# Kernel optimization log

Measured on AMD Instinct MI355X. Metric: run time of the kernel, lower is better.

## Reference

```python
import jax, jax.numpy as jnp
import numpy as np
from jax import lax

K = 3      # kernel_size
C = 64     # n_feat
B, H, W = 2, 256, 256


def _conv(x, w, b, pad):
    # NCHW conv, stride 1
    out = lax.conv_general_dilated(x, w, (1, 1), [(pad, pad), (pad, pad)],
                                   dimension_numbers=('NCHW', 'OIHW', 'NCHW'))
    return out + b[None, :, None, None]


def _prelu(x, a):
    # nn.PReLU() with a single shared learnable slope (init 0.25)
    return jnp.where(x >= 0, x, a * x)


def setup_inputs():
    key = jax.random.key(0)
    ks = jax.random.split(key, 20)
    s = 0.05
    def w(k, shape):
        return jax.random.normal(k, shape, jnp.float32) * s
    inp = {
        'image': jax.random.normal(ks[0], (B, C, H, W), jnp.float32),
        'guidance': jax.random.normal(ks[1], (B, C, H, W), jnp.float32),
        # self.tensor: 1x1 conv (2C -> C) + PReLU (shared with jbf_conv's act)
        'tensor_w': w(ks[2], (C, 2 * C, 1, 1)),
        'tensor_b': jnp.zeros((C,), jnp.float32),
        'a_jbf': jnp.full((1,), 0.25, jnp.float32),
        'kg_w1': w(ks[3], (C, C, 3, 3)), 'kg_b1': jnp.zeros((C,), jnp.float32),
        'kg_w2': w(ks[4], (C, C, 3, 3)), 'kg_b2': jnp.zeros((C,), jnp.float32),
        'kg_w3': w(ks[5], (C, C, 3, 3)), 'kg_b3': jnp.zeros((C,), jnp.float32),
        'kg_w4': w(ks[6], (C, C, 3, 3)), 'kg_b4': jnp.zeros((C,), jnp.float32),
        'kg_w5': w(ks[7], (K * K * C, C, 1, 1)),
        'kg_b5': jnp.zeros((K * K * C,), jnp.float32),
        'a_kg': jnp.full((1,), 0.25, jnp.float32),
        # jbf_conv: 3x3 C->C, PReLU (shared a_jbf), 3x3 C->C
        'jbf_w1': w(ks[8], (C, C, 3, 3)), 'jbf_b1': jnp.zeros((C,), jnp.float32),
        'jbf_w2': w(ks[9], (C, C, 3, 3)), 'jbf_b2': jnp.zeros((C,), jnp.float32),
    }
    return inp


def reference(image, guidance, tensor_w, tensor_b, a_jbf,
              kg_w1, kg_b1, kg_w2, kg_b2, kg_w3, kg_b3, kg_w4, kg_b4,
              kg_w5, kg_b5, a_kg, jbf_w1, jbf_b1, jbf_w2, jbf_b2):
    b, c, h, w = image.shape
    # fuse target+guidance features
    t = _prelu(_conv(jnp.concatenate([image, guidance], axis=1), tensor_w, tensor_b, 0), a_jbf)
    # concat_kg: predict per-pixel dynamic kernel (b, K*K*c, h, w)
    y = t
    for wt, bs in ((kg_w1, kg_b1), (kg_w2, kg_b2), (kg_w3, kg_b3), (kg_w4, kg_b4)):
        y = _prelu(_conv(y, wt, bs, 1), a_kg)
    bi_kernel = _conv(y, kg_w5, kg_b5, 0)
    # unfold: torch layout is channel-major (c, ki, kj) along dim 1
    p = (K - 1) // 2
    xp = jnp.pad(image, ((0, 0), (0, 0), (p, p), (p, p)))
    taps = [xp[:, :, i:i + h, j:j + w] for i in range(K) for j in range(K)]
    patch = jnp.stack(taps, axis=2).reshape(b, c * K * K, h, w)
    # NOTE: faithful to source -- (c*K*K) flat layout reinterpreted as (K*K, c)
    jbf = (patch * bi_kernel).reshape(b, K * K, c, h, w).sum(axis=1)
    out = _conv(_prelu(_conv(jbf, jbf_w1, jbf_b1, 1), a_jbf), jbf_w2, jbf_b2, 1)
    return out + image
```

## Files before the change

kernel.cpp:

```cpp
#include <hip/hip_runtime.h>

#define HW 65536

typedef __bf16 bf16x8 __attribute__((ext_vector_type(8)));
typedef float f32x16 __attribute__((ext_vector_type(16)));

__device__ inline unsigned short f2bf(float x) {
    union { float f; unsigned u; } v; v.f = x;
    unsigned r = v.u + 0x7FFF + ((v.u >> 16) & 1);
    return (unsigned short)(r >> 16);
}
__device__ inline float bfhi2f(unsigned u) {
    union { unsigned u; float f; } v; v.u = u & 0xffff0000u; return v.f;
}
__device__ inline float bflo2f(unsigned u) {
    union { unsigned u; float f; } v; v.u = u << 16; return v.f;
}

union FragU { uint4 u; bf16x8 v; };
__device__ inline bf16x8 ld_frag(const uint4* p) { FragU t; t.u = *p; return t.v; }


__global__ __launch_bounds__(256) void k_pre(
    const float* __restrict__ img, const float* __restrict__ gd,
    const float* __restrict__ w0, const float* __restrict__ w1,
    const float* __restrict__ w2, const float* __restrict__ w3,
    const float* __restrict__ w4, const float* __restrict__ w5,
    const float* __restrict__ w5c, const float* __restrict__ tw,
    unsigned short* __restrict__ imgT, unsigned short* __restrict__ gdT,
    unsigned short* __restrict__ wT)
{
    __shared__ float sT[64 * 66];
    int tid = threadIdx.x;
    int y = blockIdx.y;
    if (y < 4) {
        int z = y;
        int b = z & 1;
        const float* src = (z >> 1) ? gd : img;
        unsigned short* dst = (z >> 1) ? gdT : imgT;
        int px0 = blockIdx.x * 64;
        size_t sbase = (size_t)b * 64 * HW + px0;

#pragma unroll
        for (int i = 0; i < 4; ++i) {
            int e = i * 256 + tid;
            int ic = e >> 4, seg = e & 15;
            float4 v = *(const float4*)(src + sbase + (size_t)ic * HW + seg * 4);
            float* p = &sT[ic * 66 + seg * 4];
            ((float2*)p)[0] = make_float2(v.x, v.y);
            ((float2*)p)[1] = make_float2(v.z, v.w);
        }
        __syncthreads();

        size_t dbase = (size_t)b * HW * 64 + (size_t)px0 * 64;
#pragma unroll
        for (int k = 0; k < 2; ++k) {
            int idx = k * 256 + tid;
            int px = idx >> 3, u = idx & 7;
            union { uint4 q; unsigned short h[8]; } o;
#pragma unroll
            for (int j = 0; j < 8; ++j)
                o.h[j] = f2bf(sT[(u * 8 + j) * 66 + px]);
            *(uint4*)(dst + dbase + (size_t)px * 64 + u * 8) = o.q;
        }
    } else {
        int y2 = y - 4;
        unsigned short* o = wT + (size_t)y2 * 36864;
        int e = blockIdx.x * 256 + tid;
        if (y2 < 6) {
            const float* ws_[6] = {w0, w1, w2, w3, w4, w5};
            const float* w = ws_[y2];
            if (e < 36864) {
                int tap = e >> 12, oc = (e >> 6) & 63, ic = e & 63;
                int igg = ic >> 3, j = ic & 7;
                int dst = ((tap * 8 + igg) * 64 + oc) * 8 + j;
                o[dst] = f2bf(w[(oc * 64 + ic) * 9 + tap]);
            }
        } else if (y2 == 6) {
            if (e < 36864) o[e] = f2bf(w5c[e]);
        } else {
            if (e < 8192) {
                int oc = e >> 7, ic = e & 127;
                int kg = ic >> 3, j = ic & 7;
                o[((kg * 64 + oc) << 3) + j] = f2bf(tw[e]);
            }
        }
    }
}

__global__ __launch_bounds__(256, 2) void k_fuse3(
    const unsigned short* __restrict__ imgT, const unsigned short* __restrict__ gdT,
    const unsigned short* __restrict__ wTf,
    const unsigned short* __restrict__ w1T, const unsigned short* __restrict__ w2T,
    const float* __restrict__ tb, const float* __restrict__ b1,
    const float* __restrict__ b2, const float* __restrict__ ajbf,
    const float* __restrict__ akg, unsigned short* __restrict__ out)
{
    __shared__ __align__(16) char smem[54528];
    float* sB = (float*)(smem + 53760);
    uint4* sS0 = (uint4*)smem;
    uint4* sS1 = (uint4*)(smem + 19200);

    int tid = threadIdx.x;
    int wv = tid >> 6, lane = tid & 63;
    int half = lane >> 5, l31 = lane & 31;
    int w2 = wv >> 1, g = wv & 1;
    int lin = blockIdx.x + (blockIdx.y << 4) + (blockIdx.z << 9);
    int slab = lin & 7, sub = lin >> 3;
    int b = slab >> 2;
    int y0 = (slab & 3) * 64 + (sub >> 4) * 8;
    int x0 = (sub & 15) * 16;
    const size_t zbase = (size_t)b * HW * 64;
    const uint4* wgf = (const uint4*)wTf;
    const uint4* wg1 = (const uint4*)w1T;
    const uint4* wg2 = (const uint4*)w2T;

    if (tid < 64) sB[tid] = tb[tid];
    else if (tid < 128) sB[tid] = b1[tid - 64];
    else if (tid < 192) sB[tid] = b2[tid - 128];

    auto loadS = [&](int t, int h, uint4* rx) {
        const unsigned short* src = t ? gdT : imgT;
#pragma unroll
        for (int i = 0; i < 4; ++i) {
            int e = i * 256 + tid;
            int cell = e >> 2, ig = e & 3;
            int r = cell / 20, c2 = cell - r * 20;
            int gy = y0 - 2 + r, gx = x0 - 2 + c2;
            rx[i] = make_uint4(0, 0, 0, 0);
            if (e < 960 && gy >= 0 && gy < 256 && gx >= 0 && gx < 256)
                rx[i] = *(const uint4*)(src + zbase + ((size_t)(gy * 256 + gx)) * 64 + h * 32 + ig * 8);
        }
    };
    auto writeS = [&](uint4* s, const uint4* rx) {
#pragma unroll
        for (int i = 0; i < 4; ++i) {
            int e = i * 256 + tid;
            if (e < 960) s[(e >> 2) * 5 + (e & 3)] = rx[i];
        }
    };

    int cell0[4];
#pragma unroll
    for (int s = 0; s < 4; ++s) {
        int c = g * 128 + s * 32 + l31;
        cell0[s] = c < 240 ? c : 239;
    }
    f32x16 acc0[4];
#pragma unroll
    for (int s = 0; s < 4; ++s)
#pragma unroll
        for (int r = 0; r < 16; ++r) acc0[s][r] = 0.f;

    auto mm1 = [&](int t, int h, const uint4* sS) {
#pragma unroll
        for (int c = 0; c < 2; ++c) {
            int ig = c * 2 + half;
            int kg = t * 8 + h * 4 + ig;
            bf16x8 af = ld_frag(&wgf[kg * 64 + w2 * 32 + l31]);
#pragma unroll
            for (int s = 0; s < 4; ++s) {
                bf16x8 bb = ld_frag(&sS[cell0[s] * 5 + ig]);
                acc0[s] = __builtin_amdgcn_mfma_f32_32x32x16_bf16(af, bb, acc0[s], 0, 0, 0);
            }
        }
    };

    uint4 rx[4];
    loadS(0, 0, rx);
    writeS(sS0, rx);
    loadS(0, 1, rx);
    __syncthreads();
    mm1(0, 0, sS0);
    writeS(sS1, rx);
    loadS(1, 0, rx);
    __syncthreads();
    mm1(0, 1, sS1);
    writeS(sS0, rx);
    loadS(1, 1, rx);
    __syncthreads();
    mm1(1, 0, sS0);
    writeS(sS1, rx);
    __syncthreads();
    mm1(1, 1, sS1);

    float s_jbf = ajbf[0], s_kg = akg[0];
    __syncthreads();
    unsigned short* sC0 = (unsigned short*)smem;
#pragma unroll
    for (int s = 0; s < 4; ++s) {
        int cell = g * 128 + s * 32 + l31;
        if (cell < 240) {
            int R = cell / 20, C = cell - R * 20;
            int gy = y0 - 2 + R, gx = x0 - 2 + C;
            bool inb = (gy >= 0 && gy < 256 && gx >= 0 && gx < 256);
#pragma unroll
            for (int q2 = 0; q2 < 4; ++q2) {
                unsigned short hw[4];
#pragma unroll
                for (int j = 0; j < 4; ++j) {
                    int r = (q2 << 2) | j;
                    int oc = w2 * 32 + j + 8 * q2 + 4 * half;
                    float v = acc0[s][r] + sB[oc];
                    v = (v >= 0.f) ? v : s_jbf * v;
                    if (!inb) v = 0.f;
                    hw[j] = f2bf(v);
                }
                int up = (w2 * 4 + q2) ^ (cell & 7);
                *(uint2*)&sC0[cell * 64 + up * 8 + half * 4] =
                    make_uint2((unsigned)hw[0] | ((unsigned)hw[1] << 16),
                               (unsigned)hw[2] | ((unsigned)hw[3] << 16));
            }
        }
    }
    __syncthreads();

    int cellv[3], ibv[3];
#pragma unroll
    for (int s = 0; s < 3; ++s) {
        int c = g * 96 + s * 32 + l31;
        cellv[s] = c;
        int cc = c < 180 ? c : 179;
        ibv[s] = (cc / 18) * 20 + (cc % 18);
    }
    f32x16 acc1[3];
#pragma unroll
    for (int s = 0; s < 3; ++s)
#pragma unroll
        for (int r = 0; r < 16; ++r) acc1[s][r] = 0.f;

    {
        const uint4* sC04 = (const uint4*)smem;
#pragma unroll
        for (int dy = 0; dy < 3; ++dy) {
#pragma unroll
            for (int dx = 0; dx < 3; ++dx) {
                int tap = dy * 3 + dx;
                int doff = dy * 20 + dx;
#pragma unroll
                for (int c4 = 0; c4 < 4; ++c4) {
                    int unit = c4 * 2 + half;
                    bf16x8 af = ld_frag(&wg1[(tap * 8 + unit) * 64 + w2 * 32 + l31]);
#pragma unroll
                    for (int s = 0; s < 3; ++s) {
                        int cc = ibv[s] + doff;
                        bf16x8 bb = ld_frag(&sC04[cc * 8 + (unit ^ (cc & 7))]);
                        acc1[s] = __builtin_amdgcn_mfma_f32_32x32x16_bf16(af, bb, acc1[s], 0, 0, 0);
                    }
                }
            }
        }
    }

    unsigned short* sC1 = (unsigned short*)(smem + 30720);
#pragma unroll
    for (int s = 0; s < 3; ++s) {
        int cell = cellv[s];
        if (cell < 180) {
            int orow = cell / 18, ocol = cell - orow * 18;
            int gy = y0 - 1 + orow, gx = x0 - 1 + ocol;
            bool inb = (gy >= 0 && gy < 256 && gx >= 0 && gx < 256);
#pragma unroll
            for (int q2 = 0; q2 < 4; ++q2) {
                unsigned short hw[4];
#pragma unroll
                for (int j = 0; j < 4; ++j) {
                    int r = (q2 << 2) | j;
                    int oc = w2 * 32 + j + 8 * q2 + 4 * half;
                    float v = acc1[s][r] + sB[64 + oc];
                    v = (v >= 0.f) ? v : s_kg * v;
                    if (!inb) v = 0.f;
                    hw[j] = f2bf(v);
                }
                int up = (w2 * 4 + q2) ^ (cell & 7);
                *(uint2*)&sC1[cell * 64 + up * 8 + half * 4] =
                    make_uint2((unsigned)hw[0] | ((unsigned)hw[1] << 16),
                               (unsigned)hw[2] | ((unsigned)hw[3] << 16));
            }
        }
    }
    __syncthreads();

    f32x16 acc2[2];
#pragma unroll
    for (int s = 0; s < 2; ++s)
#pragma unroll
        for (int r = 0; r < 16; ++r) acc2[s][r] = 0.f;

    int rowS[2], colS[2];
#pragma unroll
    for (int s = 0; s < 2; ++s) {
        int px = g * 64 + s * 32 + l31;
        rowS[s] = px >> 4; colS[s] = px & 15;
    }
    {
        const uint4* sC14 = (const uint4*)(smem + 30720);
#pragma unroll
        for (int dy = 0; dy < 3; ++dy) {
#pragma unroll
            for (int dx = 0; dx < 3; ++dx) {
                int tap = dy * 3 + dx;
#pragma unroll
                for (int c = 0; c < 4; ++c) {
                    int ig = c * 2 + half;
                    bf16x8 af = ld_frag(&wg2[(tap * 8 + ig) * 64 + w2 * 32 + l31]);
#pragma unroll
                    for (int s = 0; s < 2; ++s) {
                        int cl = (rowS[s] + dy) * 18 + colS[s] + dx;
                        bf16x8 bb = ld_frag(&sC14[cl * 8 + (ig ^ (cl & 7))]);
                        acc2[s] = __builtin_amdgcn_mfma_f32_32x32x16_bf16(af, bb, acc2[s], 0, 0, 0);
                    }
                }
            }
        }
    }

    unsigned short* sT16 = (unsigned short*)smem;
#pragma unroll
    for (int s = 0; s < 2; ++s) {
        int px = g * 64 + s * 32 + l31;
#pragma unroll
        for (int q2 = 0; q2 < 4; ++q2) {
            unsigned short hw[4];
#pragma unroll
            for (int j = 0; j < 4; ++j) {
                int r = (q2 << 2) | j;
                int oc = w2 * 32 + j + 8 * q2 + 4 * half;
                float v = acc2[s][r] + sB[128 + oc];
                v = (v >= 0.f) ? v : s_kg * v;
                hw[j] = f2bf(v);
            }
            int up = (w2 * 4 + q2) ^ (px & 7);
            uint2* p = (uint2*)&sT16[px * 64 + up * 8 + half * 4];
            *p = make_uint2((unsigned)hw[0] | ((unsigned)hw[1] << 16),
                            (unsigned)hw[2] | ((unsigned)hw[3] << 16));
        }
    }
    __syncthreads();
#pragma unroll
    for (int k = 0; k < 4; ++k) {
        int idx = k * 256 + tid;
        int row = idx >> 7, rem = idx & 127;
        int col = rem >> 3, u = rem & 7;
        int px = row * 16 + col;
        uint4 v = *(uint4*)&sT16[px * 64 + (u ^ (px & 7)) * 8];
        *(uint4*)(out + zbase + ((size_t)((y0 + row) * 256 + x0 + col)) * 64 + u * 8) = v;
    }
}

#define XU 5

template<int MODE>
__global__ __launch_bounds__(256, 4) void k_conv2x(
    const unsigned short* __restrict__ in,
    const unsigned short* __restrict__ w1T, const unsigned short* __restrict__ w2T,
    const float* __restrict__ b1, const float* __restrict__ b2,
    const float* __restrict__ a, const float* __restrict__ res,
    void* __restrict__ outv)
{
    __shared__ __align__(16) char smem[38912];
    uint4* sIn0 = (uint4*)smem;
    uint4* sIn1 = (uint4*)(smem + 19200);
    float* sB = (float*)(smem + 38400);

    int tid = threadIdx.x;
    int wv = tid >> 6, lane = tid & 63;
    int half = lane >> 5, l31 = lane & 31;
    int w2 = wv >> 1, g = wv & 1;
    int lin = blockIdx.x + (blockIdx.y << 4) + (blockIdx.z << 9);
    int slab = lin & 7, sub = lin >> 3;
    int b = slab >> 2;
    int y0 = (slab & 3) * 64 + (sub >> 4) * 8;
    int x0 = (sub & 15) * 16;
    const size_t zbase = (size_t)b * HW * 64;
    const uint4* wg1 = (const uint4*)w1T;
    const uint4* wg2 = (const uint4*)w2T;

    if (tid < 64) sB[tid] = b1[tid];
    else if (tid < 128) sB[tid] = b2[tid - 64];

    auto loadIn = [&](int h, uint4* rx) {
#pragma unroll
        for (int i = 0; i < 4; ++i) {
            int e = i * 256 + tid;
            int cell = e >> 2, ig = e & 3;
            int r = cell / 20, c2 = cell - r * 20;
            int gy = y0 - 2 + r, gx = x0 - 2 + c2;
            rx[i] = make_uint4(0, 0, 0, 0);
            bool act = (i < 3) || (e < 960);
            if (act && gy >= 0 && gy < 256 && gx >= 0 && gx < 256)
                rx[i] = *(const uint4*)(in + zbase + ((size_t)(gy * 256 + gx)) * 64 + h * 32 + ig * 8);
        }
    };
    auto writeIn = [&](uint4* s, const uint4* rx) {
#pragma unroll
        for (int i = 0; i < 4; ++i) {
            int e = i * 256 + tid;
            if (i < 3 || e < 960) s[(e >> 2) * XU + (e & 3)] = rx[i];
        }
    };

    int cellv[3], ibv[3];
#pragma unroll
    for (int s = 0; s < 3; ++s) {
        int c = g * 96 + s * 32 + l31;
        cellv[s] = c;
        int cc = c < 180 ? c : 179;
        ibv[s] = (cc / 18) * 20 + (cc % 18);
    }

    f32x16 acc1[3];
#pragma unroll
    for (int s = 0; s < 3; ++s)
#pragma unroll
        for (int r = 0; r < 16; ++r) acc1[s][r] = 0.f;

    auto conv1_h = [&](int h, const uint4* sInp) {
#pragma unroll
        for (int dy = 0; dy < 3; ++dy) {
#pragma unroll
            for (int dx = 0; dx < 3; ++dx) {
                int tap = dy * 3 + dx;
                int doff = dy * 20 + dx;
#pragma unroll
                for (int c = 0; c < 2; ++c) {
                    int ig = c * 2 + half;
                    bf16x8 af = ld_frag(&wg1[(tap * 8 + h * 4 + ig) * 64 + w2 * 32 + l31]);
#pragma unroll
                    for (int s = 0; s < 3; ++s) {
                        bf16x8 bb = ld_frag(&sInp[(ibv[s] + doff) * XU + ig]);
                        acc1[s] = __builtin_amdgcn_mfma_f32_32x32x16_bf16(af, bb, acc1[s], 0, 0, 0);
                    }
                }
            }
        }
    };

    uint4 rx[4];
    loadIn(0, rx);
    writeIn(sIn0, rx);
    uint4 ry[4];
    loadIn(1, ry);
    __syncthreads();
    conv1_h(0, sIn0);
    writeIn(sIn1, ry);
    __syncthreads();
    conv1_h(1, sIn1);

    float s1 = a[0];
    __syncthreads();
    unsigned short* sC16 = (unsigned short*)smem;
#pragma unroll
    for (int s = 0; s < 3; ++s) {
        int cell = cellv[s];
        if (cell < 180) {
            int orow = cell / 18, ocol = cell - orow * 18;
            int gy = y0 - 1 + orow, gx = x0 - 1 + ocol;
            bool inb = (gy >= 0 && gy < 256 && gx >= 0 && gx < 256);
#pragma unroll
            for (int q2 = 0; q2 < 4; ++q2) {
                unsigned short hw[4];
#pragma unroll
                for (int j = 0; j < 4; ++j) {
                    int r = (q2 << 2) | j;
                    int oc = w2 * 32 + j + 8 * q2 + 4 * half;
                    float v = acc1[s][r] + sB[oc];
                    v = (v >= 0.f) ? v : s1 * v;
                    if (!inb) v = 0.f;
                    hw[j] = f2bf(v);
                }
                int up = (w2 * 4 + q2) ^ (cell & 7);
                *(uint2*)&sC16[cell * 64 + up * 8 + half * 4] =
                    make_uint2((unsigned)hw[0] | ((unsigned)hw[1] << 16),
                               (unsigned)hw[2] | ((unsigned)hw[3] << 16));
            }
        }
    }
    __syncthreads();

    f32x16 acc2[2];
#pragma unroll
    for (int s = 0; s < 2; ++s)
#pragma unroll
        for (int r = 0; r < 16; ++r) acc2[s][r] = 0.f;

    int rowS[2], colS[2];
#pragma unroll
    for (int s = 0; s < 2; ++s) {
        int px = g * 64 + s * 32 + l31;
        rowS[s] = px >> 4; colS[s] = px & 15;
    }
    {
        const uint4* sC4 = (const uint4*)smem;
#pragma unroll
        for (int dy = 0; dy < 3; ++dy) {
#pragma unroll
            for (int dx = 0; dx < 3; ++dx) {
                int tap = dy * 3 + dx;
#pragma unroll
                for (int c = 0; c < 4; ++c) {
                    int ig = c * 2 + half;
                    bf16x8 af = ld_frag(&wg2[(tap * 8 + ig) * 64 + w2 * 32 + l31]);
#pragma unroll
                    for (int s = 0; s < 2; ++s) {
                        int cl = (rowS[s] + dy) * 18 + colS[s] + dx;
                        bf16x8 bb = ld_frag(&sC4[cl * 8 + (ig ^ (cl & 7))]);
                        acc2[s] = __builtin_amdgcn_mfma_f32_32x32x16_bf16(af, bb, acc2[s], 0, 0, 0);
                    }
                }
            }
        }
    }

    if (MODE == 0) {
        __syncthreads();
        unsigned short* sT16 = (unsigned short*)smem;
#pragma unroll
        for (int s = 0; s < 2; ++s) {
            int px = g * 64 + s * 32 + l31;
#pragma unroll
            for (int q2 = 0; q2 < 4; ++q2) {
                unsigned short hw[4];
#pragma unroll
                for (int j = 0; j < 4; ++j) {
                    int r = (q2 << 2) | j;
                    int oc = w2 * 32 + j + 8 * q2 + 4 * half;
                    float v = acc2[s][r] + sB[64 + oc];
                    v = (v >= 0.f) ? v : s1 * v;
                    hw[j] = f2bf(v);
                }
                int up = (w2 * 4 + q2) ^ (px & 7);
                uint2* p = (uint2*)&sT16[px * 64 + up * 8 + half * 4];
                *p = make_uint2((unsigned)hw[0] | ((unsigned)hw[1] << 16),
                                (unsigned)hw[2] | ((unsigned)hw[3] << 16));
            }
        }
        __syncthreads();
        unsigned short* outT = (unsigned short*)outv;
#pragma unroll
        for (int k = 0; k < 4; ++k) {
            int idx = k * 256 + tid;
            int row = idx >> 7, rem = idx & 127;
            int col = rem >> 3, u = rem & 7;
            int px = row * 16 + col;
            uint4 v = *(uint4*)&sT16[px * 64 + (u ^ (px & 7)) * 8];
            *(uint4*)(outT + zbase + ((size_t)((y0 + row) * 256 + x0 + col)) * 64 + u * 8) = v;
        }
    } else {
        float* outF = (float*)outv;
#pragma unroll
        for (int s = 0; s < 2; ++s) {
            int px = g * 64 + s * 32 + l31;
            int y = y0 + (px >> 4), x = x0 + (px & 15);
            size_t pbase = (size_t)b * 64 * HW + (size_t)y * 256 + x;
#pragma unroll
            for (int r = 0; r < 16; ++r) {
                int oc = w2 * 32 + (r & 3) + 8 * (r >> 2) + 4 * half;
                float v = acc2[s][r] + sB[64 + oc];
                v += res[pbase + (size_t)oc * HW];
                outF[pbase + (size_t)oc * HW] = v;
            }
        }
    }
}

struct OffTab { unsigned v[9][32]; int chlo[9]; };
constexpr OffTab make_tab() {
    OffTab t{};
    for (int kk = 0; kk < 9; ++kk) {
        int chlo = (kk * 64) / 9;
        t.chlo[kk] = chlo;
        for (int ot = 0; ot < 2; ++ot)
            for (int r = 0; r < 16; ++r) {
                int cc0 = ot * 32 + (r & 3) + 8 * (r >> 2);
                int q0 = kk * 64 + cc0, q1 = q0 + 4;
                int o0 = (q0 / 9 - chlo) * 360 + (q0 % 9 / 3) * 40 + (q0 % 9 % 3);
                int o1 = (q1 / 9 - chlo) * 360 + (q1 % 9 / 3) * 40 + (q1 % 9 % 3);
                t.v[kk][ot * 16 + r] = (unsigned)o0 | ((unsigned)o1 << 16);
            }
    }
    return t;
}
__constant__ OffTab kOff = make_tab();

__global__ __launch_bounds__(256, 2) void k_jbfm(
    const unsigned short* __restrict__ y4, const float* __restrict__ img,
    const unsigned short* __restrict__ w5T, const float* __restrict__ b5,
    unsigned short* __restrict__ out)
{
    __shared__ __align__(16) char smem[78592];
    uint4* sY = (uint4*)smem;
    float* sB5 = (float*)(smem + 76288);
    unsigned short* sT16 = (unsigned short*)smem;

    int tid = threadIdx.x;
    int wv = tid >> 6, lane = tid & 63;
    int half = lane >> 5, l31 = lane & 31;
    int lin = blockIdx.x + (blockIdx.y << 3) + (blockIdx.z << 8);
    int slab = lin & 7, sub = lin >> 3;
    int b = slab >> 2;
    int y0 = (slab & 3) * 64 + (sub >> 3) * 8;
    int x0 = (sub & 7) * 32;
    size_t zbase = (size_t)b * HW * 64;
    size_t ibase = (size_t)b * 64 * HW;

    int p_off[3], p_dst[3];
    bool p_a[3], p_b[3], p_act[3];
#pragma unroll
    for (int i = 0; i < 3; ++i) {
        int e = i * 256 + tid;
        bool act = e < 720;
        int ch = e / 90, rem = e - ch * 90;
        int rp = rem / 10, seg = rem - rp * 10;
        int gy = y0 + rp - 1;
        int gxb = x0 - 4 + seg * 4;
        bool xok = (gxb >= 0 && gxb < 256);
        p_act[i] = act;
        p_a[i] = act && xok && gy >= 0 && gy < 256;
        p_b[i] = act && xok && (gy + 1) < 256;
        p_off[i] = ch * HW + gy * 256 + gxb;
        p_dst[i] = ch * 360 + rp * 40 + seg * 4;
    }

#pragma unroll
    for (int i = 0; i < 8; ++i) {
        int e = i * 256 + tid;
        int px = e >> 3, ig = e & 7;
        int gy = y0 + (px >> 5), gx = x0 + (px & 31);
        sY[px * 9 + ig] = *(const uint4*)(y4 + zbase + ((size_t)(gy * 256 + gx)) * 64 + ig * 8);
    }
    for (int e = tid; e < 576; e += 256) sB5[e] = b5[e];

    {
        uint4* sW50 = (uint4*)(smem + 36864);
        unsigned* sP0 = (unsigned*)(smem + 53248);
#pragma unroll
        for (int u = 0; u < 2; ++u) {
            int uu = u * 256 + tid;
            int cc = uu & 63, ig = uu >> 6;
            sW50[uu] = ((const uint4*)w5T)[cc * 8 + ig];
        }
        const float* rp0 = img + ibase;
#pragma unroll
        for (int i = 0; i < 3; ++i) {
            float4 fa = make_float4(0, 0, 0, 0), fb = make_float4(0, 0, 0, 0);
            if (p_a[i]) fa = *(const float4*)(rp0 + p_off[i]);
            if (p_b[i]) fb = *(const float4*)(rp0 + p_off[i] + 256);
            if (p_act[i]) {
                uint4 pk;
                pk.x = (unsigned)f2bf(fa.x) | ((unsigned)f2bf(fb.x) << 16);
                pk.y = (unsigned)f2bf(fa.y) | ((unsigned)f2bf(fb.y) << 16);
                pk.z = (unsigned)f2bf(fa.z) | ((unsigned)f2bf(fb.z) << 16);
                pk.w = (unsigned)f2bf(fa.w) | ((unsigned)f2bf(fb.w) << 16);
                *(uint4*)&sP0[p_dst[i]] = pk;
            }
        }
    }

    float jb[2][2][16];
#pragma unroll
    for (int i = 0; i < 2; ++i)
#pragma unroll
        for (int j = 0; j < 2; ++j)
#pragma unroll
            for (int r = 0; r < 16; ++r) jb[i][j][r] = 0.f;

    __syncthreads();

#pragma unroll 1
    for (int kk = 0; kk < 9; ++kk) {
        const int cur = kk & 1;
        const uint4* sW5c = (const uint4*)(smem + 36864 + cur * 8192);
        const unsigned* sPc = (const unsigned*)(smem + 53248 + cur * 11520);

        uint4 wpre0, wpre1;
        float4 pfa[3], pfb[3];
        if (kk < 8) {
            const int nk = kk + 1;
            const int chlo_n = kOff.chlo[nk];
            {
                int cc = tid & 63, ig = tid >> 6;
                wpre0 = ((const uint4*)w5T)[(nk * 64 + cc) * 8 + ig];
                int uu = 256 + tid;
                int cc1 = uu & 63, ig1 = uu >> 6;
                wpre1 = ((const uint4*)w5T)[(nk * 64 + cc1) * 8 + ig1];
            }
            const float* rp0 = img + ibase + (size_t)chlo_n * HW;
#pragma unroll
            for (int i = 0; i < 3; ++i) {
                pfa[i] = make_float4(0, 0, 0, 0);
                pfb[i] = make_float4(0, 0, 0, 0);
                if (p_a[i]) pfa[i] = *(const float4*)(rp0 + p_off[i]);
                if (p_b[i]) pfb[i] = *(const float4*)(rp0 + p_off[i] + 256);
            }
        }

        f32x16 acc[2][2];
#pragma unroll
        for (int ot = 0; ot < 2; ++ot)
#pragma unroll
            for (int r = 0; r < 16; ++r) {
                int cc0 = ot * 32 + (r & 3) + 8 * (r >> 2);
                float bv = sB5[kk * 64 + cc0 + 4 * half];
                acc[ot][0][r] = bv;
                acc[ot][1][r] = bv;
            }

#pragma unroll
        for (int c = 0; c < 4; ++c) {
            int ig = c * 2 + half;
            bf16x8 a0 = ld_frag(&sW5c[ig * 64 + l31]);
            bf16x8 a1 = ld_frag(&sW5c[ig * 64 + 32 + l31]);
            int p0 = wv * 64 + l31;
            bf16x8 b0 = ld_frag(&sY[p0 * 9 + ig]);
            bf16x8 b1 = ld_frag(&sY[(p0 + 32) * 9 + ig]);
            acc[0][0] = __builtin_amdgcn_mfma_f32_32x32x16_bf16(a0, b0, acc[0][0], 0, 0, 0);
            acc[0][1] = __builtin_amdgcn_mfma_f32_32x32x16_bf16(a0, b1, acc[0][1], 0, 0, 0);
            acc[1][0] = __builtin_amdgcn_mfma_f32_32x32x16_bf16(a1, b0, acc[1][0], 0, 0, 0);
            acc[1][1] = __builtin_amdgcn_mfma_f32_32x32x16_bf16(a1, b1, acc[1][1], 0, 0, 0);
        }

        {
            const unsigned* basep = sPc + wv * 80 + l31 + 3;
            const unsigned* tab = kOff.v[kk];
#pragma unroll
            for (int ot = 0; ot < 2; ++ot)
#pragma unroll
                for (int r = 0; r < 16; ++r) {
                    unsigned oo = tab[ot * 16 + r];
                    unsigned o0 = oo & 0xffffu, o1 = oo >> 16;
                    unsigned pv = basep[half ? o1 : o0];
                    jb[ot][0][r] = fmaf(acc[ot][0][r], bflo2f(pv), jb[ot][0][r]);
                    jb[ot][1][r] = fmaf(acc[ot][1][r], bfhi2f(pv), jb[ot][1][r]);
                }
        }

        if (kk < 8) {
            uint4* sW5n = (uint4*)(smem + 36864 + (cur ^ 1) * 8192);
            unsigned* sPn = (unsigned*)(smem + 53248 + (cur ^ 1) * 11520);
            sW5n[tid] = wpre0;
            sW5n[256 + tid] = wpre1;
#pragma unroll
            for (int i = 0; i < 3; ++i) {
                if (p_act[i]) {
                    uint4 pk;
                    pk.x = (unsigned)f2bf(pfa[i].x) | ((unsigned)f2bf(pfb[i].x) << 16);
                    pk.y = (unsigned)f2bf(pfa[i].y) | ((unsigned)f2bf(pfb[i].y) << 16);
                    pk.z = (unsigned)f2bf(pfa[i].z) | ((unsigned)f2bf(pfb[i].z) << 16);
                    pk.w = (unsigned)f2bf(pfa[i].w) | ((unsigned)f2bf(pfb[i].w) << 16);
                    *(uint4*)&sPn[p_dst[i]] = pk;
                }
            }
        }
        __syncthreads();
    }

#pragma unroll
    for (int ot = 0; ot < 2; ++ot)
#pragma unroll
        for (int pt = 0; pt < 2; ++pt) {
            int px = wv * 64 + pt * 32 + l31;
#pragma unroll
            for (int q2 = 0; q2 < 4; ++q2) {
                unsigned short hw[4];
#pragma unroll
                for (int j = 0; j < 4; ++j) {
                    int r = (q2 << 2) | j;
                    hw[j] = f2bf(jb[ot][pt][r]);
                }
                int unit = ot * 4 + q2;
                int up = unit ^ (px & 7);
                uint2* p = (uint2*)&sT16[px * 64 + up * 8 + half * 4];
                *p = make_uint2((unsigned)hw[0] | ((unsigned)hw[1] << 16),
                                (unsigned)hw[2] | ((unsigned)hw[3] << 16));
            }
        }
    __syncthreads();
#pragma unroll
    for (int k = 0; k < 8; ++k) {
        int col = tid >> 3, u = tid & 7;
        int px = k * 32 + col;
        uint4 v = *(uint4*)&sT16[px * 64 + (u ^ (px & 7)) * 8];
        *(uint4*)(out + zbase + ((size_t)((y0 + k) * 256 + x0 + col)) * 64 + u * 8) = v;
    }
}

extern "C" void kernel_launch(void* const* d_in, const int* in_sizes, int n_in,
                              void* d_out, int out_size, void* d_ws, size_t ws_size,
                              hipStream_t stream) {
    const float* img  = (const float*)d_in[0];
    const float* gd   = (const float*)d_in[1];
    const float* tw   = (const float*)d_in[2];
    const float* tb   = (const float*)d_in[3];
    const float* ajbf = (const float*)d_in[4];
    const float* kw1  = (const float*)d_in[5];
    const float* kb1  = (const float*)d_in[6];
    const float* kw2  = (const float*)d_in[7];
    const float* kb2  = (const float*)d_in[8];
    const float* kw3  = (const float*)d_in[9];
    const float* kb3  = (const float*)d_in[10];
    const float* kw4  = (const float*)d_in[11];
    const float* kb4  = (const float*)d_in[12];
    const float* kw5  = (const float*)d_in[13];
    const float* kb5  = (const float*)d_in[14];
    const float* akg  = (const float*)d_in[15];
    const float* jw1  = (const float*)d_in[16];
    const float* jb1  = (const float*)d_in[17];
    const float* jw2  = (const float*)d_in[18];
    const float* jb2  = (const float*)d_in[19];
    float* out  = (float*)d_out;

    const size_t TEN = (size_t)2 * HW * 64;
    unsigned short* bufA = (unsigned short*)d_ws;
    unsigned short* imgT = bufA + TEN;
    unsigned short* gdT  = imgT + TEN;
    unsigned short* wT   = gdT + TEN;
    unsigned short* bufB = (unsigned short*)d_out;
    unsigned short* bufC = gdT;

    dim3 gs(16, 32, 2);
    dim3 gw(8, 32, 2);

    k_pre<<<dim3(1024, 12), 256, 0, stream>>>(img, gd, kw1, kw2, kw3, kw4,
                                              jw1, jw2, kw5, tw, imgT, gdT, wT);

    k_fuse3<<<gs, 256, 0, stream>>>(imgT, gdT, wT + (size_t)7 * 36864,
                                    wT + (size_t)0 * 36864, wT + (size_t)1 * 36864,
                                    tb, kb1, kb2, ajbf, akg, bufA);

    k_conv2x<0><<<gs, 256, 0, stream>>>(bufA, wT + (size_t)2 * 36864, wT + (size_t)3 * 36864,
                                        kb3, kb4, akg, nullptr, bufB);

    k_jbfm<<<gw, 256, 0, stream>>>(bufB, img, wT + (size_t)6 * 36864, kb5, bufC);

    k_conv2x<2><<<gs, 256, 0, stream>>>(bufC, wT + (size_t)4 * 36864, wT + (size_t)5 * 36864,
                                        jb1, jb2, ajbf, img, out);
}
```

Measured before the change: 288.9 us.

## Fuse kg conv3/conv4 pair into the dynamic-kernel JBF kernel

```diff
diff --git a/kernel.cpp b/kernel.cpp
--- a/kernel.cpp
+++ b/kernel.cpp
@@ -583,19 +583,26 @@
 }
 __constant__ OffTab kOff = make_tab();
 
-__global__ __launch_bounds__(256, 2) void k_jbfm(
-    const unsigned short* __restrict__ y4, const float* __restrict__ img,
-    const unsigned short* __restrict__ w5T, const float* __restrict__ b5,
+__global__ __launch_bounds__(256, 2) void k_jbfm5(
+    const unsigned short* __restrict__ in, const float* __restrict__ img,
+    const unsigned short* __restrict__ w1T, const unsigned short* __restrict__ w2T,
+    const unsigned short* __restrict__ w5T,
+    const float* __restrict__ b1, const float* __restrict__ b2,
+    const float* __restrict__ b5, const float* __restrict__ akg,
     unsigned short* __restrict__ out)
 {
-    __shared__ __align__(16) char smem[78592];
-    uint4* sY = (uint4*)smem;
-    float* sB5 = (float*)(smem + 76288);
+    __shared__ __align__(16) char smem[80896];
+    float* sB = (float*)(smem + 80384);
+    uint4* sIn0 = (uint4*)smem;
+    uint4* sIn1 = (uint4*)(smem + 34560);
+    uint4* sY = (uint4*)(smem + 43520);
+    float* sB5 = (float*)(smem + 39424);
     unsigned short* sT16 = (unsigned short*)smem;
 
     int tid = threadIdx.x;
     int wv = tid >> 6, lane = tid & 63;
     int half = lane >> 5, l31 = lane & 31;
+    int w2 = wv >> 1, g = wv & 1;
     int lin = blockIdx.x + (blockIdx.y << 3) + (blockIdx.z << 8);
     int slab = lin & 7, sub = lin >> 3;
     int b = slab >> 2;
@@ -603,6 +610,168 @@
     int x0 = (sub & 7) * 32;
     size_t zbase = (size_t)b * HW * 64;
     size_t ibase = (size_t)b * 64 * HW;
+    const uint4* wg1 = (const uint4*)w1T;
+    const uint4* wg2 = (const uint4*)w2T;
+
+    if (tid < 64) sB[tid] = b1[tid];
+    else if (tid < 128) sB[tid] = b2[tid - 64];
+
+    auto loadIn = [&](int h, uint4* rx) {
+#pragma unroll
+        for (int i = 0; i < 7; ++i) {
+            int e = i * 256 + tid;
+            int cell = e >> 2, ig = e & 3;
+            int r = cell / 36, c2 = cell - r * 36;
+            int gy = y0 - 2 + r, gx = x0 - 2 + c2;
+            rx[i] = make_uint4(0, 0, 0, 0);
+            if (e < 1728 && gy >= 0 && gy < 256 && gx >= 0 && gx < 256)
+                rx[i] = *(const uint4*)(in + zbase + ((size_t)(gy * 256 + gx)) * 64 + h * 32 + ig * 8);
+        }
+    };
+    auto writeIn = [&](uint4* s, const uint4* rx) {
+#pragma unroll
+        for (int i = 0; i < 7; ++i) {
+            int e = i * 256 + tid;
+            if (e < 1728) s[(e >> 2) * XU + (e & 3)] = rx[i];
+        }
+    };
+
+    int cellv[6], ibv[6];
+    bool val[6];
+#pragma unroll
+    for (int s = 0; s < 6; ++s) {
+        int c = g * 170 + s * 32 + l31;
+        val[s] = (s * 32 + l31) < 170;
+        cellv[s] = c;
+        int cc = c < 340 ? c : 339;
+        ibv[s] = (cc / 34) * 36 + (cc % 34);
+    }
+    f32x16 acc1[6];
+#pragma unroll
+    for (int s = 0; s < 6; ++s)
+#pragma unroll
+        for (int r = 0; r < 16; ++r) acc1[s][r] = 0.f;
+
+    auto conv1_h = [&](int h, const uint4* sInp) {
+#pragma unroll
+        for (int dy = 0; dy < 3; ++dy) {
+#pragma unroll
+            for (int dx = 0; dx < 3; ++dx) {
+                int tap = dy * 3 + dx;
+                int doff = dy * 36 + dx;
+#pragma unroll
+                for (int c = 0; c < 2; ++c) {
+                    int ig = c * 2 + half;
+                    bf16x8 af = ld_frag(&wg1[(tap * 8 + h * 4 + ig) * 64 + w2 * 32 + l31]);
+#pragma unroll
+                    for (int s = 0; s < 6; ++s) {
+                        bf16x8 bb = ld_frag(&sInp[(ibv[s] + doff) * XU + ig]);
+                        acc1[s] = __builtin_amdgcn_mfma_f32_32x32x16_bf16(af, bb, acc1[s], 0, 0, 0);
+                    }
+                }
+            }
+        }
+    };
+
+    uint4 rx[7], ry[7];
+    loadIn(0, rx);
+    writeIn(sIn0, rx);
+    loadIn(1, ry);
+    __syncthreads();
+    conv1_h(0, sIn0);
+    writeIn(sIn1, ry);
+    __syncthreads();
+    conv1_h(1, sIn1);
+
+    float s_kg = akg[0];
+    __syncthreads();
+    unsigned short* sC16 = (unsigned short*)smem;
+#pragma unroll
+    for (int s = 0; s < 6; ++s) {
+        if (val[s]) {
+            int cell = cellv[s];
+            int row = cell / 34, col = cell - row * 34;
+            int gy = y0 - 1 + row, gx = x0 - 1 + col;
+            bool inb = (gy >= 0 && gy < 256 && gx >= 0 && gx < 256);
+#pragma unroll
+            for (int q2 = 0; q2 < 4; ++q2) {
+                unsigned short hw[4];
+#pragma unroll
+                for (int j = 0; j < 4; ++j) {
+                    int r = (q2 << 2) | j;
+                    int oc = w2 * 32 + j + 8 * q2 + 4 * half;
+                    float v = acc1[s][r] + sB[oc];
+                    v = (v >= 0.f) ? v : s_kg * v;
+                    if (!inb) v = 0.f;
+                    hw[j] = f2bf(v);
+                }
+                int up = (w2 * 4 + q2) ^ (cell & 7);
+                *(uint2*)&sC16[cell * 64 + up * 8 + half * 4] =
+                    make_uint2((unsigned)hw[0] | ((unsigned)hw[1] << 16),
+                               (unsigned)hw[2] | ((unsigned)hw[3] << 16));
+            }
+        }
+    }
+    __syncthreads();
+
+    f32x16 acc2[4];
+#pragma unroll
+    for (int s = 0; s < 4; ++s)
+#pragma unroll
+        for (int r = 0; r < 16; ++r) acc2[s][r] = 0.f;
+
+    int rowS[4], colS[4];
+#pragma unroll
+    for (int s = 0; s < 4; ++s) {
+        int p = g * 128 + s * 32 + l31;
+        rowS[s] = p >> 5; colS[s] = p & 31;
+    }
+    {
+        const uint4* sC4 = (const uint4*)smem;
+#pragma unroll
+        for (int dy = 0; dy < 3; ++dy) {
+#pragma unroll
+            for (int dx = 0; dx < 3; ++dx) {
+                int tap = dy * 3 + dx;
+#pragma unroll
+                for (int c = 0; c < 4; ++c) {
+                    int ig = c * 2 + half;
+                    bf16x8 af = ld_frag(&wg2[(tap * 8 + ig) * 64 + w2 * 32 + l31]);
+#pragma unroll
+                    for (int s = 0; s < 4; ++s) {
+                        int cl = (rowS[s] + dy) * 34 + colS[s] + dx;
+                        bf16x8 bb = ld_frag(&sC4[cl * 8 + (ig ^ (cl & 7))]);
+                        acc2[s] = __builtin_amdgcn_mfma_f32_32x32x16_bf16(af, bb, acc2[s], 0, 0, 0);
+                    }
+                }
+            }
+        }
+    }
+
+    {
+        unsigned short* sY16 = (unsigned short*)(smem + 43520);
+#pragma unroll
+        for (int s = 0; s < 4; ++s) {
+            int px = g * 128 + s * 32 + l31;
+#pragma unroll
+            for (int q2 = 0; q2 < 4; ++q2) {
+                int ig = w2 * 4 + q2;
+                unsigned short hw[4];
+#pragma unroll
+                for (int j = 0; j < 4; ++j) {
+                    int r = (q2 << 2) | j;
+                    int oc = w2 * 32 + j + 8 * q2 + 4 * half;
+                    float v = acc2[s][r] + sB[64 + oc];
+                    v = (v >= 0.f) ? v : s_kg * v;
+                    hw[j] = f2bf(v);
+                }
+                *(uint2*)&sY16[px * 72 + ig * 8 + half * 4] =
+                    make_uint2((unsigned)hw[0] | ((unsigned)hw[1] << 16),
+                               (unsigned)hw[2] | ((unsigned)hw[3] << 16));
+            }
+        }
+    }
+    __syncthreads();
 
     int p_off[3], p_dst[3];
     bool p_a[3], p_b[3], p_act[3];
@@ -622,18 +791,11 @@
         p_dst[i] = ch * 360 + rp * 40 + seg * 4;
     }
 
-#pragma unroll
-    for (int i = 0; i < 8; ++i) {
-        int e = i * 256 + tid;
-        int px = e >> 3, ig = e & 7;
-        int gy = y0 + (px >> 5), gx = x0 + (px & 31);
-        sY[px * 9 + ig] = *(const uint4*)(y4 + zbase + ((size_t)(gy * 256 + gx)) * 64 + ig * 8);
-    }
     for (int e = tid; e < 576; e += 256) sB5[e] = b5[e];
 
     {
-        uint4* sW50 = (uint4*)(smem + 36864);
-        unsigned* sP0 = (unsigned*)(smem + 53248);
+        uint4* sW50 = (uint4*)smem;
+        unsigned* sP0 = (unsigned*)(smem + 16384);
 #pragma unroll
         for (int u = 0; u < 2; ++u) {
             int uu = u * 256 + tid;
@@ -670,8 +832,8 @@
 #pragma unroll 1
     for (int kk = 0; kk < 9; ++kk) {
         const int cur = kk & 1;
-        const uint4* sW5c = (const uint4*)(smem + 36864 + cur * 8192);
-        const unsigned* sPc = (const unsigned*)(smem + 53248 + cur * 11520);
+        const uint4* sW5c = (const uint4*)(smem + cur * 8192);
+        const unsigned* sPc = (const unsigned*)(smem + 16384 + cur * 11520);
 
         uint4 wpre0, wpre1;
         float4 pfa[3], pfb[3];
@@ -736,8 +898,8 @@
         }
 
         if (kk < 8) {
-            uint4* sW5n = (uint4*)(smem + 36864 + (cur ^ 1) * 8192);
-            unsigned* sPn = (unsigned*)(smem + 53248 + (cur ^ 1) * 11520);
+            uint4* sW5n = (uint4*)(smem + (cur ^ 1) * 8192);
+            unsigned* sPn = (unsigned*)(smem + 16384 + (cur ^ 1) * 11520);
             sW5n[tid] = wpre0;
             sW5n[256 + tid] = wpre1;
 #pragma unroll
@@ -815,7 +977,6 @@
     unsigned short* imgT = bufA + TEN;
     unsigned short* gdT  = imgT + TEN;
     unsigned short* wT   = gdT + TEN;
-    unsigned short* bufB = (unsigned short*)d_out;
     unsigned short* bufC = gdT;
 
     dim3 gs(16, 32, 2);
@@ -828,10 +989,10 @@
                                     wT + (size_t)0 * 36864, wT + (size_t)1 * 36864,
                                     tb, kb1, kb2, ajbf, akg, bufA);
 
-    k_conv2x<0><<<gs, 256, 0, stream>>>(bufA, wT + (size_t)2 * 36864, wT + (size_t)3 * 36864,
-                                        kb3, kb4, akg, nullptr, bufB);
-
-    k_jbfm<<<gw, 256, 0, stream>>>(bufB, img, wT + (size_t)6 * 36864, kb5, bufC);
+    k_jbfm5<<<gw, 256, 0, stream>>>(bufA, img,
+                                    wT + (size_t)2 * 36864, wT + (size_t)3 * 36864,
+                                    wT + (size_t)6 * 36864,
+                                    kb3, kb4, kb5, akg, bufC);
 
     k_conv2x<2><<<gs, 256, 0, stream>>>(bufC, wT + (size_t)4 * 36864, wT + (size_t)5 * 36864,
                                         jb1, jb2, ajbf, img, out);
```

Result: faster. 282.9 us (-2.1%).
